# Performance work log

Hardware: AMD Instinct MI355X
Metric: run time of the kernel (lower is better)

The kernel has to match this reference:

```python
import jax, jax.numpy as jnp
import numpy as np

N = 50000      # num nodes
HID = 64       # hidden_dim
N2V = 64       # node2vec dim
E = 800000     # num edges
EP = 100000    # prediction edges
L = 2          # num_layers
EPS = 1e-5     # BatchNorm eps


def setup_inputs() -> dict:
    key = jax.random.key(0)
    ks = jax.random.split(key, 8)
    edge_index = jax.random.randint(ks[0], (2, E), 0, N)
    pred_edge = jax.random.randint(ks[1], (EP, 2), 0, N)
    id_emb = jax.random.normal(ks[2], (N, HID), jnp.float32) * 0.1      # learnable ID embedding
    n2v_emb = jax.random.normal(ks[3], (N, N2V), jnp.float32) * 0.1     # frozen node2vec embedding
    proj_w = jax.random.normal(ks[4], (HID + N2V, HID), jnp.float32) / np.sqrt(HID + N2V)
    proj_b = jnp.zeros((HID,), jnp.float32)
    conv_w = jax.random.normal(ks[5], (L, HID, HID), jnp.float32) / np.sqrt(HID)
    conv_b = jnp.zeros((L, HID), jnp.float32)
    bn_gamma = jnp.ones((L, HID), jnp.float32)
    bn_beta = jnp.zeros((L, HID), jnp.float32)
    return {"edge_index": edge_index, "pred_edge": pred_edge, "id_emb": id_emb,
            "n2v_emb": n2v_emb, "proj_w": proj_w, "proj_b": proj_b,
            "conv_w": conv_w, "conv_b": conv_b, "bn_gamma": bn_gamma, "bn_beta": bn_beta}


def reference(edge_index, pred_edge, id_emb, n2v_emb, proj_w, proj_b, conv_w, conv_b, bn_gamma, bn_beta):
    # input projection of concatenated embeddings: [N, HID+N2V] @ [HID+N2V, HID]
    x = jnp.concatenate([id_emb, n2v_emb], axis=1) @ proj_w + proj_b

    # GCN normalization with self-loops: norm_e = d^-1/2[src] * d^-1/2[dst]
    loops = jnp.arange(N, dtype=edge_index.dtype)
    row = jnp.concatenate([edge_index[0], loops])   # source nodes
    col = jnp.concatenate([edge_index[1], loops])   # destination nodes
    deg = jax.ops.segment_sum(jnp.ones(row.shape, x.dtype), col, num_segments=N)
    dis = jnp.where(deg > 0, jax.lax.rsqrt(deg), 0.0)
    norm = dis[row] * dis[col]                      # [E+N]

    for l in range(L):
        h = x @ conv_w[l]                                                    # [N, HID]
        agg = jax.ops.segment_sum(norm[:, None] * h[row], col, num_segments=N) + conv_b[l]
        # BatchNorm1d (training-mode batch stats over nodes)
        mu = agg.mean(axis=0)
        var = agg.var(axis=0)
        xn = (agg - mu) * jax.lax.rsqrt(var + EPS) * bn_gamma[l] + bn_beta[l]
        x = x + jax.nn.relu(xn)                                              # residual (shapes match)

    # dot-product link decoder
    z = x
    return (z[pred_edge[:, 0]] * z[pred_edge[:, 1]]).sum(axis=1)
```

## Files before the change

kernel.cpp:

```cpp
#include <hip/hip_runtime.h>

#define NN 50000
#define HID 64
#define NE 800000
#define NP 100000
#define BN_EPS 1e-5f
#define NB1 196

static inline size_t alignup(size_t x) { return (x + 255) & ~(size_t)255; }

__device__ __forceinline__ void f4fma(float a, const float4& w, float4& c) {
    c.x += a * w.x; c.y += a * w.y; c.z += a * w.z; c.w += a * w.w;
}
__device__ __forceinline__ void f4add(const float4& a, float4& c) {
    c.x += a.x; c.y += a.y; c.z += a.z; c.w += a.w;
}
__device__ __forceinline__ unsigned bfpack(float a, float b) {
    unsigned ua = __float_as_uint(a), ub = __float_as_uint(b);
    ua = (ua + 0x7fffu + ((ua >> 16) & 1u)) >> 16;
    ub = (ub + 0x7fffu + ((ub >> 16) & 1u)) >> 16;
    return ua | (ub << 16);
}
__device__ __forceinline__ float4 bf2f4(uint2 u) {
    float4 r;
    r.x = __uint_as_float(u.x << 16);
    r.y = __uint_as_float(u.x & 0xffff0000u);
    r.z = __uint_as_float(u.y << 16);
    r.w = __uint_as_float(u.y & 0xffff0000u);
    return r;
}


__global__ __launch_bounds__(256) void k_zero(int* __restrict__ cnt, float* __restrict__ sums,
                                              int* __restrict__ cursor) {
    int i = blockIdx.x * blockDim.x + threadIdx.x;
    if (i < NN) cnt[i] = 0;
    if (i < 256) sums[i] = 0.f;
    if (i == 0) *cursor = 0;
}


__global__ __launch_bounds__(256) void k_count(const int* __restrict__ col,
                                               int* __restrict__ cnt, int* __restrict__ rank) {
    int e = blockIdx.x * blockDim.x + threadIdx.x;
    if (e < NE) rank[e] = atomicAdd(&cnt[col[e]], 1);
}


__global__ __launch_bounds__(256) void k_alloc(const int* __restrict__ cnt,
                                               int* __restrict__ offs,
                                               float* __restrict__ dis,
                                               int* __restrict__ cursor) {
    __shared__ int s[256];
    __shared__ int base;
    int t = threadIdx.x;
    int i = blockIdx.x * 256 + t;
    int v = (i < NN) ? cnt[i] : 0;
    if (i < NN) dis[i] = rsqrtf((float)(v + 1));
    int va = (v + 7) & ~7;
    s[t] = va;
    __syncthreads();
    for (int off = 1; off < 256; off <<= 1) {
        int add = (t >= off) ? s[t - off] : 0;
        __syncthreads();
        s[t] += add;
        __syncthreads();
    }
    if (t == 255) base = atomicAdd(cursor, s[255]);
    __syncthreads();
    if (i < NN) offs[i] = base + s[t] - va;
}


__global__ __launch_bounds__(256) void k_fill(const int* __restrict__ row, const int* __restrict__ col,
                                              const int* __restrict__ rank, const int* __restrict__ offs,
                                              unsigned short* __restrict__ csr) {
    int e = blockIdx.x * blockDim.x + threadIdx.x;
    if (e >= NE) return;
    csr[offs[col[e]] + rank[e]] = (unsigned short)row[e];
}


__global__ __launch_bounds__(256) void k_proj(const float* __restrict__ id_emb,
                                              const float* __restrict__ n2v,
                                              const float* __restrict__ W,
                                              const float* __restrict__ b,
                                              const float* __restrict__ dis,
                                              float* __restrict__ x,
                                              unsigned short* __restrict__ xh) {
    __shared__ unsigned short Wlh[128 * 64];
    __shared__ unsigned short Al[32 * 132];
    int tid = threadIdx.x;
    int node0 = blockIdx.x * 32;
    const float2* W2f = (const float2*)W;
#pragma unroll
    for (int it = 0; it < 16; ++it) {
        int i = it * 256 + tid;
        float2 w = W2f[i];
        *(unsigned*)&Wlh[2 * i] = bfpack(w.x, w.y);
    }
    const float2* id2 = (const float2*)id_emb;
    const float2* nv2 = (const float2*)n2v;
#pragma unroll
    for (int it = 0; it < 8; ++it) {
        int i = it * 256 + tid;
        int r = i >> 6, kp = i & 63;
        int n = node0 + r;
        float2 v = make_float2(0.f, 0.f);
        if (n < NN) v = (kp < 32) ? id2[n * 32 + kp] : nv2[n * 32 + (kp - 32)];
        *(unsigned*)&Al[r * 132 + 2 * kp] = bfpack(v.x, v.y);
    }
    __syncthreads();
    int sub = tid >> 4, q = tid & 15;
    const uint2* W2 = (const uint2*)Wlh;
    float4* x4 = (float4*)x;
    uint2* xh2 = (uint2*)xh;
    float4 bb = ((const float4*)b)[q];
    float4 c0 = bb, c1 = bb;
#pragma unroll 4
    for (int k4 = 0; k4 < 32; ++k4) {
        float4 w0 = bf2f4(W2[(k4 * 4 + 0) * 16 + q]);
        float4 w1 = bf2f4(W2[(k4 * 4 + 1) * 16 + q]);
        float4 w2 = bf2f4(W2[(k4 * 4 + 2) * 16 + q]);
        float4 w3 = bf2f4(W2[(k4 * 4 + 3) * 16 + q]);
        float4 a0 = bf2f4(*(const uint2*)&Al[(sub * 2 + 0) * 132 + k4 * 4]);
        float4 a1 = bf2f4(*(const uint2*)&Al[(sub * 2 + 1) * 132 + k4 * 4]);
        f4fma(a0.x, w0, c0); f4fma(a0.y, w1, c0); f4fma(a0.z, w2, c0); f4fma(a0.w, w3, c0);
        f4fma(a1.x, w0, c1); f4fma(a1.y, w1, c1); f4fma(a1.z, w2, c1); f4fma(a1.w, w3, c1);
    }
    int n0 = node0 + sub * 2;
    if (n0 + 0 < NN) { float d = dis[n0+0]; x4[(n0+0)*16+q] = c0;
        xh2[(n0+0)*16+q] = make_uint2(bfpack(c0.x*d,c0.y*d), bfpack(c0.z*d,c0.w*d)); }
    if (n0 + 1 < NN) { float d = dis[n0+1]; x4[(n0+1)*16+q] = c1;
        xh2[(n0+1)*16+q] = make_uint2(bfpack(c1.x*d,c1.y*d), bfpack(c1.z*d,c1.w*d)); }
}


__global__ __launch_bounds__(256) void k_gather(const int* __restrict__ offs,
                                                const int* __restrict__ cnt,
                                                const unsigned short* __restrict__ csr,
                                                const float* __restrict__ dis,
                                                const unsigned short* __restrict__ xh,
                                                unsigned short* __restrict__ th) {
    int gw = (blockIdx.x * blockDim.x + threadIdx.x) >> 6;
    int lane = threadIdx.x & 63;
    int sub = lane >> 4, q = lane & 15;
    int node = gw * 4 + sub;
    if (node >= NN) return;
    const uint2* xh2 = (const uint2*)xh;
    float4 acc = make_float4(0.f, 0.f, 0.f, 0.f);
    const unsigned short* cs = csr + offs[node];
    int c = cnt[node];
    int jj = 0;
    for (; jj + 7 < c; jj += 8) {
        uint4 s8 = *(const uint4*)(cs + jj);
        int s0 = s8.x & 0xffff, s1 = s8.x >> 16;
        int s2 = s8.y & 0xffff, s3 = s8.y >> 16;
        int s4 = s8.z & 0xffff, s5 = s8.z >> 16;
        int s6 = s8.w & 0xffff, s7 = s8.w >> 16;
        uint2 u0 = xh2[s0 * 16 + q];
        uint2 u1 = xh2[s1 * 16 + q];
        uint2 u2 = xh2[s2 * 16 + q];
        uint2 u3 = xh2[s3 * 16 + q];
        uint2 u4 = xh2[s4 * 16 + q];
        uint2 u5 = xh2[s5 * 16 + q];
        uint2 u6 = xh2[s6 * 16 + q];
        uint2 u7 = xh2[s7 * 16 + q];
        f4add(bf2f4(u0), acc); f4add(bf2f4(u1), acc);
        f4add(bf2f4(u2), acc); f4add(bf2f4(u3), acc);
        f4add(bf2f4(u4), acc); f4add(bf2f4(u5), acc);
        f4add(bf2f4(u6), acc); f4add(bf2f4(u7), acc);
    }
    for (; jj < c; ++jj) {
        uint2 u0 = xh2[cs[jj] * 16 + q];
        f4add(bf2f4(u0), acc);
    }
    f4add(bf2f4(xh2[node * 16 + q]), acc);
    float di = dis[node];
    acc.x *= di; acc.y *= di; acc.z *= di; acc.w *= di;
    ((uint2*)th)[node * 16 + q] = make_uint2(bfpack(acc.x, acc.y), bfpack(acc.z, acc.w));
}


__global__ __launch_bounds__(256) void k_gemm_stats(const unsigned short* __restrict__ th,
                                                    const float* __restrict__ W,
                                                    float* __restrict__ agg,
                                                    float* __restrict__ sums) {
    __shared__ float Wl[64 * 64];
    __shared__ float ls0[16][64];
    __shared__ float ls1[16][64];
    int tid = threadIdx.x;
    for (int i = tid; i < 64 * 64; i += 256) Wl[i] = W[i];
    __syncthreads();
    int sub = tid >> 4, q = tid & 15;
    const uint2* t2 = (const uint2*)th;
    const float4* W4 = (const float4*)Wl;
    float4* agg4 = (float4*)agg;
    float4 s1 = make_float4(0.f, 0.f, 0.f, 0.f), s2 = s1;
    const int ngroups = (NN + 63) / 64;
    for (int g = blockIdx.x; g < ngroups; g += gridDim.x) {
        int n0 = g * 64 + sub * 4;
        int r0 = min(n0 + 0, NN - 1), r1 = min(n0 + 1, NN - 1);
        int r2 = min(n0 + 2, NN - 1), r3 = min(n0 + 3, NN - 1);
        float4 c0 = make_float4(0.f,0.f,0.f,0.f), c1 = c0, c2 = c0, c3 = c0;
#pragma unroll 4
        for (int k4 = 0; k4 < 16; ++k4) {
            float4 a0 = bf2f4(t2[r0 * 16 + k4]);
            float4 a1 = bf2f4(t2[r1 * 16 + k4]);
            float4 a2 = bf2f4(t2[r2 * 16 + k4]);
            float4 a3 = bf2f4(t2[r3 * 16 + k4]);
            float4 w0 = W4[(k4 * 4 + 0) * 16 + q];
            float4 w1 = W4[(k4 * 4 + 1) * 16 + q];
            float4 w2 = W4[(k4 * 4 + 2) * 16 + q];
            float4 w3 = W4[(k4 * 4 + 3) * 16 + q];
            f4fma(a0.x, w0, c0); f4fma(a0.y, w1, c0); f4fma(a0.z, w2, c0); f4fma(a0.w, w3, c0);
            f4fma(a1.x, w0, c1); f4fma(a1.y, w1, c1); f4fma(a1.z, w2, c1); f4fma(a1.w, w3, c1);
            f4fma(a2.x, w0, c2); f4fma(a2.y, w1, c2); f4fma(a2.z, w2, c2); f4fma(a2.w, w3, c2);
            f4fma(a3.x, w0, c3); f4fma(a3.y, w1, c3); f4fma(a3.z, w2, c3); f4fma(a3.w, w3, c3);
        }
        if (n0 + 0 < NN) { agg4[(n0 + 0) * 16 + q] = c0;
            s1.x += c0.x; s1.y += c0.y; s1.z += c0.z; s1.w += c0.w;
            s2.x += c0.x*c0.x; s2.y += c0.y*c0.y; s2.z += c0.z*c0.z; s2.w += c0.w*c0.w; }
        if (n0 + 1 < NN) { agg4[(n0 + 1) * 16 + q] = c1;
            s1.x += c1.x; s1.y += c1.y; s1.z += c1.z; s1.w += c1.w;
            s2.x += c1.x*c1.x; s2.y += c1.y*c1.y; s2.z += c1.z*c1.z; s2.w += c1.w*c1.w; }
        if (n0 + 2 < NN) { agg4[(n0 + 2) * 16 + q] = c2;
            s1.x += c2.x; s1.y += c2.y; s1.z += c2.z; s1.w += c2.w;
            s2.x += c2.x*c2.x; s2.y += c2.y*c2.y; s2.z += c2.z*c2.z; s2.w += c2.w*c2.w; }
        if (n0 + 3 < NN) { agg4[(n0 + 3) * 16 + q] = c3;
            s1.x += c3.x; s1.y += c3.y; s1.z += c3.z; s1.w += c3.w;
            s2.x += c3.x*c3.x; s2.y += c3.y*c3.y; s2.z += c3.z*c3.z; s2.w += c3.w*c3.w; }
    }
    ls0[sub][q * 4 + 0] = s1.x; ls0[sub][q * 4 + 1] = s1.y;
    ls0[sub][q * 4 + 2] = s1.z; ls0[sub][q * 4 + 3] = s1.w;
    ls1[sub][q * 4 + 0] = s2.x; ls1[sub][q * 4 + 1] = s2.y;
    ls1[sub][q * 4 + 2] = s2.z; ls1[sub][q * 4 + 3] = s2.w;
    __syncthreads();
    if (tid < 64) {
        float a = 0.f;
#pragma unroll
        for (int r = 0; r < 16; ++r) a += ls0[r][tid];
        atomicAdd(&sums[tid], a);
    } else if (tid < 128) {
        int c = tid - 64;
        float a = 0.f;
#pragma unroll
        for (int r = 0; r < 16; ++r) a += ls1[r][c];
        atomicAdd(&sums[64 + c], a);
    }
}


__global__ __launch_bounds__(256) void k_bnupdate(const float* __restrict__ agg,
                                                  const float* __restrict__ sums,
                                                  const float* __restrict__ gamma,
                                                  const float* __restrict__ beta,
                                                  const float* __restrict__ dis,
                                                  int prescale,
                                                  float* __restrict__ x,
                                                  unsigned short* __restrict__ xh) {
    int i = blockIdx.x * blockDim.x + threadIdx.x;
    if (i >= NN * 16) return;
    int f4 = i & 15;
    const float invn = 1.0f / (float)NN;
    float4 sm = ((const float4*)sums)[f4];
    float4 sq = ((const float4*)(sums + 64))[f4];
    float4 g = ((const float4*)gamma)[f4];
    float4 be = ((const float4*)beta)[f4];
    float4 a = ((const float4*)agg)[i];
    float4 xv = ((const float4*)x)[i];
    float mu, var, rstd, xn;
    mu = sm.x * invn; var = sq.x * invn - mu * mu; rstd = rsqrtf(var + BN_EPS);
    xn = (a.x - mu) * rstd * g.x + be.x; xv.x += fmaxf(xn, 0.f);
    mu = sm.y * invn; var = sq.y * invn - mu * mu; rstd = rsqrtf(var + BN_EPS);
    xn = (a.y - mu) * rstd * g.y + be.y; xv.y += fmaxf(xn, 0.f);
    mu = sm.z * invn; var = sq.z * invn - mu * mu; rstd = rsqrtf(var + BN_EPS);
    xn = (a.z - mu) * rstd * g.z + be.z; xv.z += fmaxf(xn, 0.f);
    mu = sm.w * invn; var = sq.w * invn - mu * mu; rstd = rsqrtf(var + BN_EPS);
    xn = (a.w - mu) * rstd * g.w + be.w; xv.w += fmaxf(xn, 0.f);
    ((float4*)x)[i] = xv;
    float d = prescale ? dis[i >> 4] : 1.0f;
    ((uint2*)xh)[i] = make_uint2(bfpack(xv.x * d, xv.y * d), bfpack(xv.z * d, xv.w * d));
}


__global__ __launch_bounds__(256) void k_decode(const int* __restrict__ pred,
                                                const unsigned short* __restrict__ zh,
                                                float* __restrict__ out) {
    int gw = (blockIdx.x * blockDim.x + threadIdx.x) >> 6;
    int lane = threadIdx.x & 63;
    int sub = lane >> 4, q = lane & 15;
    int p = gw * 4 + sub;
    if (p >= NP) return;
    const uint2* z2 = (const uint2*)zh;
    int a = pred[2 * p], b = pred[2 * p + 1];
    float4 va = bf2f4(z2[a * 16 + q]);
    float4 vb = bf2f4(z2[b * 16 + q]);
    float v = va.x * vb.x + va.y * vb.y + va.z * vb.z + va.w * vb.w;
    v += __shfl_xor(v, 1);
    v += __shfl_xor(v, 2);
    v += __shfl_xor(v, 4);
    v += __shfl_xor(v, 8);
    if (q == 0) out[p] = v;
}

extern "C" void kernel_launch(void* const* d_in, const int* in_sizes, int n_in,
                              void* d_out, int out_size, void* d_ws, size_t ws_size,
                              hipStream_t stream) {
    const int* edge_index = (const int*)d_in[0];
    const int* pred       = (const int*)d_in[1];
    const float* id_emb   = (const float*)d_in[2];
    const float* n2v      = (const float*)d_in[3];
    const float* proj_w   = (const float*)d_in[4];
    const float* proj_b   = (const float*)d_in[5];
    const float* conv_w   = (const float*)d_in[6];
    const float* gamma    = (const float*)d_in[8];
    const float* beta     = (const float*)d_in[9];
    float* out = (float*)d_out;

    char* ws = (char*)d_ws;
    size_t off = 0;
    float* dis   = (float*)(ws + off); off += alignup(NN * 4);
    int* cnt     = (int*)(ws + off);   off += alignup(NN * 4);
    int* offs    = (int*)(ws + off);   off += alignup(NN * 4);
    int* rank    = (int*)(ws + off);   off += alignup((size_t)NE * 4);
    int* cursor  = (int*)(ws + off);   off += alignup(4);
    unsigned short* csr = (unsigned short*)(ws + off); off += alignup((size_t)(NE + NN * 8) * 2);
    float* x     = (float*)(ws + off); off += alignup((size_t)NN * 64 * 4);
    float* agg   = (float*)(ws + off); off += alignup((size_t)NN * 64 * 4);
    unsigned short* xh = (unsigned short*)(ws + off); off += alignup((size_t)NN * 64 * 2);
    unsigned short* th = (unsigned short*)(ws + off); off += alignup((size_t)NN * 64 * 2);
    float* sums  = (float*)(ws + off);

    const int* row = edge_index;
    const int* col = edge_index + NE;

    k_zero<<<NB1, 256, 0, stream>>>(cnt, sums, cursor);
    k_count<<<(NE + 255) / 256, 256, 0, stream>>>(col, cnt, rank);
    k_alloc<<<NB1, 256, 0, stream>>>(cnt, offs, dis, cursor);
    k_fill<<<(NE + 255) / 256, 256, 0, stream>>>(row, col, rank, offs, csr);

    k_proj<<<(NN + 31) / 32, 256, 0, stream>>>(id_emb, n2v, proj_w, proj_b, dis, x, xh);

    for (int l = 0; l < 2; ++l) {
        k_gather<<<((NN + 3) / 4 * 64 + 255) / 256, 256, 0, stream>>>(offs, cnt, csr, dis, xh, th);
        k_gemm_stats<<<512, 256, 0, stream>>>(th, conv_w + l * 64 * 64, agg, sums + l * 128);
        k_bnupdate<<<(NN * 16 + 255) / 256, 256, 0, stream>>>(agg, sums + l * 128, gamma + l * 64,
                                                              beta + l * 64, dis, (l == 0) ? 1 : 0, x, xh);
    }

    k_decode<<<(NP / 4 * 64 + 255) / 256, 256, 0, stream>>>(pred, xh, out);
}
```

Baseline: 201.7 us.

## Fuse GEMM, BatchNorm stats and update via grid-wide barrier

Merges the GEMM+stats kernel and the BN update kernel into one. It launches one block per 64-node group (782 blocks) and uses an atomic counter spin barrier so that all blocks wait for the global column sums before applying BatchNorm. The GEMM results stay in registers, which removes the fp32 agg buffer write and read and one kernel launch per layer. The cost is the grid-wide barrier. It deadlocks unless all 782 blocks are co-resident, so the code depends on occupancy (launch_bounds 256,4) and has no fallback.

```diff
diff --git a/kernel.cpp b/kernel.cpp
--- a/kernel.cpp
+++ b/kernel.cpp
@@ -6,6 +6,7 @@
 #define NP 100000
 #define BN_EPS 1e-5f
 #define NB1 196
+#define NGRP ((NN + 63) / 64)
 
 static inline size_t alignup(size_t x) { return (x + 255) & ~(size_t)255; }
 
@@ -32,11 +33,12 @@
 
 
 __global__ __launch_bounds__(256) void k_zero(int* __restrict__ cnt, float* __restrict__ sums,
-                                              int* __restrict__ cursor) {
+                                              int* __restrict__ cursor, unsigned* __restrict__ done) {
     int i = blockIdx.x * blockDim.x + threadIdx.x;
     if (i < NN) cnt[i] = 0;
     if (i < 256) sums[i] = 0.f;
     if (i == 0) *cursor = 0;
+    if (i < 2) done[i] = 0u;
 }
 
 
@@ -182,10 +184,16 @@
 }
 
 
-__global__ __launch_bounds__(256) void k_gemm_stats(const unsigned short* __restrict__ th,
-                                                    const float* __restrict__ W,
-                                                    float* __restrict__ agg,
-                                                    float* __restrict__ sums) {
+__global__ __launch_bounds__(256, 4) void k_gemmbn(const unsigned short* __restrict__ th,
+                                                   const float* __restrict__ W,
+                                                   float* __restrict__ sums,
+                                                   unsigned* __restrict__ done,
+                                                   const float* __restrict__ gamma,
+                                                   const float* __restrict__ beta,
+                                                   const float* __restrict__ dis,
+                                                   int prescale,
+                                                   float* __restrict__ x,
+                                                   unsigned short* __restrict__ xh) {
     __shared__ float Wl[64 * 64];
     __shared__ float ls0[16][64];
     __shared__ float ls1[16][64];
@@ -195,42 +203,34 @@
     int sub = tid >> 4, q = tid & 15;
     const uint2* t2 = (const uint2*)th;
     const float4* W4 = (const float4*)Wl;
-    float4* agg4 = (float4*)agg;
-    float4 s1 = make_float4(0.f, 0.f, 0.f, 0.f), s2 = s1;
-    const int ngroups = (NN + 63) / 64;
-    for (int g = blockIdx.x; g < ngroups; g += gridDim.x) {
-        int n0 = g * 64 + sub * 4;
-        int r0 = min(n0 + 0, NN - 1), r1 = min(n0 + 1, NN - 1);
-        int r2 = min(n0 + 2, NN - 1), r3 = min(n0 + 3, NN - 1);
-        float4 c0 = make_float4(0.f,0.f,0.f,0.f), c1 = c0, c2 = c0, c3 = c0;
+    int n0 = blockIdx.x * 64 + sub * 4;
+    int r0 = min(n0 + 0, NN - 1), r1 = min(n0 + 1, NN - 1);
+    int r2 = min(n0 + 2, NN - 1), r3 = min(n0 + 3, NN - 1);
+    float4 c0 = make_float4(0.f,0.f,0.f,0.f), c1 = c0, c2 = c0, c3 = c0;
 #pragma unroll 4
-        for (int k4 = 0; k4 < 16; ++k4) {
-            float4 a0 = bf2f4(t2[r0 * 16 + k4]);
-            float4 a1 = bf2f4(t2[r1 * 16 + k4]);
-            float4 a2 = bf2f4(t2[r2 * 16 + k4]);
-            float4 a3 = bf2f4(t2[r3 * 16 + k4]);
-            float4 w0 = W4[(k4 * 4 + 0) * 16 + q];
-            float4 w1 = W4[(k4 * 4 + 1) * 16 + q];
-            float4 w2 = W4[(k4 * 4 + 2) * 16 + q];
-            float4 w3 = W4[(k4 * 4 + 3) * 16 + q];
-            f4fma(a0.x, w0, c0); f4fma(a0.y, w1, c0); f4fma(a0.z, w2, c0); f4fma(a0.w, w3, c0);
-            f4fma(a1.x, w0, c1); f4fma(a1.y, w1, c1); f4fma(a1.z, w2, c1); f4fma(a1.w, w3, c1);
-            f4fma(a2.x, w0, c2); f4fma(a2.y, w1, c2); f4fma(a2.z, w2, c2); f4fma(a2.w, w3, c2);
-            f4fma(a3.x, w0, c3); f4fma(a3.y, w1, c3); f4fma(a3.z, w2, c3); f4fma(a3.w, w3, c3);
-        }
-        if (n0 + 0 < NN) { agg4[(n0 + 0) * 16 + q] = c0;
-            s1.x += c0.x; s1.y += c0.y; s1.z += c0.z; s1.w += c0.w;
-            s2.x += c0.x*c0.x; s2.y += c0.y*c0.y; s2.z += c0.z*c0.z; s2.w += c0.w*c0.w; }
-        if (n0 + 1 < NN) { agg4[(n0 + 1) * 16 + q] = c1;
-            s1.x += c1.x; s1.y += c1.y; s1.z += c1.z; s1.w += c1.w;
-            s2.x += c1.x*c1.x; s2.y += c1.y*c1.y; s2.z += c1.z*c1.z; s2.w += c1.w*c1.w; }
-        if (n0 + 2 < NN) { agg4[(n0 + 2) * 16 + q] = c2;
-            s1.x += c2.x; s1.y += c2.y; s1.z += c2.z; s1.w += c2.w;
-            s2.x += c2.x*c2.x; s2.y += c2.y*c2.y; s2.z += c2.z*c2.z; s2.w += c2.w*c2.w; }
-        if (n0 + 3 < NN) { agg4[(n0 + 3) * 16 + q] = c3;
-            s1.x += c3.x; s1.y += c3.y; s1.z += c3.z; s1.w += c3.w;
-            s2.x += c3.x*c3.x; s2.y += c3.y*c3.y; s2.z += c3.z*c3.z; s2.w += c3.w*c3.w; }
-    }
+    for (int k4 = 0; k4 < 16; ++k4) {
+        float4 a0 = bf2f4(t2[r0 * 16 + k4]);
+        float4 a1 = bf2f4(t2[r1 * 16 + k4]);
+        float4 a2 = bf2f4(t2[r2 * 16 + k4]);
+        float4 a3 = bf2f4(t2[r3 * 16 + k4]);
+        float4 w0 = W4[(k4 * 4 + 0) * 16 + q];
+        float4 w1 = W4[(k4 * 4 + 1) * 16 + q];
+        float4 w2 = W4[(k4 * 4 + 2) * 16 + q];
+        float4 w3 = W4[(k4 * 4 + 3) * 16 + q];
+        f4fma(a0.x, w0, c0); f4fma(a0.y, w1, c0); f4fma(a0.z, w2, c0); f4fma(a0.w, w3, c0);
+        f4fma(a1.x, w0, c1); f4fma(a1.y, w1, c1); f4fma(a1.z, w2, c1); f4fma(a1.w, w3, c1);
+        f4fma(a2.x, w0, c2); f4fma(a2.y, w1, c2); f4fma(a2.z, w2, c2); f4fma(a2.w, w3, c2);
+        f4fma(a3.x, w0, c3); f4fma(a3.y, w1, c3); f4fma(a3.z, w2, c3); f4fma(a3.w, w3, c3);
+    }
+    float4 s1 = make_float4(0.f,0.f,0.f,0.f), s2 = s1;
+    if (n0 + 0 < NN) { s1.x += c0.x; s1.y += c0.y; s1.z += c0.z; s1.w += c0.w;
+        s2.x += c0.x*c0.x; s2.y += c0.y*c0.y; s2.z += c0.z*c0.z; s2.w += c0.w*c0.w; }
+    if (n0 + 1 < NN) { s1.x += c1.x; s1.y += c1.y; s1.z += c1.z; s1.w += c1.w;
+        s2.x += c1.x*c1.x; s2.y += c1.y*c1.y; s2.z += c1.z*c1.z; s2.w += c1.w*c1.w; }
+    if (n0 + 2 < NN) { s1.x += c2.x; s1.y += c2.y; s1.z += c2.z; s1.w += c2.w;
+        s2.x += c2.x*c2.x; s2.y += c2.y*c2.y; s2.z += c2.z*c2.z; s2.w += c2.w*c2.w; }
+    if (n0 + 3 < NN) { s1.x += c3.x; s1.y += c3.y; s1.z += c3.z; s1.w += c3.w;
+        s2.x += c3.x*c3.x; s2.y += c3.y*c3.y; s2.z += c3.z*c3.z; s2.w += c3.w*c3.w; }
     ls0[sub][q * 4 + 0] = s1.x; ls0[sub][q * 4 + 1] = s1.y;
     ls0[sub][q * 4 + 2] = s1.z; ls0[sub][q * 4 + 3] = s1.w;
     ls1[sub][q * 4 + 0] = s2.x; ls1[sub][q * 4 + 1] = s2.y;
@@ -248,39 +248,50 @@
         for (int r = 0; r < 16; ++r) a += ls1[r][c];
         atomicAdd(&sums[64 + c], a);
     }
-}
-
-
-__global__ __launch_bounds__(256) void k_bnupdate(const float* __restrict__ agg,
-                                                  const float* __restrict__ sums,
-                                                  const float* __restrict__ gamma,
-                                                  const float* __restrict__ beta,
-                                                  const float* __restrict__ dis,
-                                                  int prescale,
-                                                  float* __restrict__ x,
-                                                  unsigned short* __restrict__ xh) {
-    int i = blockIdx.x * blockDim.x + threadIdx.x;
-    if (i >= NN * 16) return;
-    int f4 = i & 15;
+    __syncthreads();
+    if (tid == 0) {
+        __threadfence();
+        __hip_atomic_fetch_add(done, 1u, __ATOMIC_ACQ_REL, __HIP_MEMORY_SCOPE_AGENT);
+        while (__hip_atomic_load(done, __ATOMIC_ACQUIRE, __HIP_MEMORY_SCOPE_AGENT) < (unsigned)NGRP)
+            __builtin_amdgcn_s_sleep(8);
+    }
+    __syncthreads();
     const float invn = 1.0f / (float)NN;
-    float4 sm = ((const float4*)sums)[f4];
-    float4 sq = ((const float4*)(sums + 64))[f4];
-    float4 g = ((const float4*)gamma)[f4];
-    float4 be = ((const float4*)beta)[f4];
-    float4 a = ((const float4*)agg)[i];
-    float4 xv = ((const float4*)x)[i];
-    float mu, var, rstd, xn;
-    mu = sm.x * invn; var = sq.x * invn - mu * mu; rstd = rsqrtf(var + BN_EPS);
-    xn = (a.x - mu) * rstd * g.x + be.x; xv.x += fmaxf(xn, 0.f);
-    mu = sm.y * invn; var = sq.y * invn - mu * mu; rstd = rsqrtf(var + BN_EPS);
-    xn = (a.y - mu) * rstd * g.y + be.y; xv.y += fmaxf(xn, 0.f);
-    mu = sm.z * invn; var = sq.z * invn - mu * mu; rstd = rsqrtf(var + BN_EPS);
-    xn = (a.z - mu) * rstd * g.z + be.z; xv.z += fmaxf(xn, 0.f);
-    mu = sm.w * invn; var = sq.w * invn - mu * mu; rstd = rsqrtf(var + BN_EPS);
-    xn = (a.w - mu) * rstd * g.w + be.w; xv.w += fmaxf(xn, 0.f);
-    ((float4*)x)[i] = xv;
-    float d = prescale ? dis[i >> 4] : 1.0f;
-    ((uint2*)xh)[i] = make_uint2(bfpack(xv.x * d, xv.y * d), bfpack(xv.z * d, xv.w * d));
+    float mu0, mu1, mu2, mu3, rs0, rs1, rs2, rs3, sm, sq, var;
+    sm = __hip_atomic_load(&sums[q * 4 + 0], __ATOMIC_RELAXED, __HIP_MEMORY_SCOPE_AGENT);
+    sq = __hip_atomic_load(&sums[64 + q * 4 + 0], __ATOMIC_RELAXED, __HIP_MEMORY_SCOPE_AGENT);
+    mu0 = sm * invn; var = sq * invn - mu0 * mu0; rs0 = rsqrtf(var + BN_EPS);
+    sm = __hip_atomic_load(&sums[q * 4 + 1], __ATOMIC_RELAXED, __HIP_MEMORY_SCOPE_AGENT);
+    sq = __hip_atomic_load(&sums[64 + q * 4 + 1], __ATOMIC_RELAXED, __HIP_MEMORY_SCOPE_AGENT);
+    mu1 = sm * invn; var = sq * invn - mu1 * mu1; rs1 = rsqrtf(var + BN_EPS);
+    sm = __hip_atomic_load(&sums[q * 4 + 2], __ATOMIC_RELAXED, __HIP_MEMORY_SCOPE_AGENT);
+    sq = __hip_atomic_load(&sums[64 + q * 4 + 2], __ATOMIC_RELAXED, __HIP_MEMORY_SCOPE_AGENT);
+    mu2 = sm * invn; var = sq * invn - mu2 * mu2; rs2 = rsqrtf(var + BN_EPS);
+    sm = __hip_atomic_load(&sums[q * 4 + 3], __ATOMIC_RELAXED, __HIP_MEMORY_SCOPE_AGENT);
+    sq = __hip_atomic_load(&sums[64 + q * 4 + 3], __ATOMIC_RELAXED, __HIP_MEMORY_SCOPE_AGENT);
+    mu3 = sm * invn; var = sq * invn - mu3 * mu3; rs3 = rsqrtf(var + BN_EPS);
+    float4 g4 = ((const float4*)gamma)[q];
+    float4 be4 = ((const float4*)beta)[q];
+    float4* x4 = (float4*)x;
+    uint2* xh2 = (uint2*)xh;
+#define BN_ROW(ci, idx)                                                                 \
+    if (n0 + idx < NN) {                                                                \
+        float4 xv = x4[(n0 + idx) * 16 + q];                                            \
+        float xn;                                                                       \
+        xn = (ci.x - mu0) * rs0 * g4.x + be4.x; xv.x += fmaxf(xn, 0.f);                 \
+        xn = (ci.y - mu1) * rs1 * g4.y + be4.y; xv.y += fmaxf(xn, 0.f);                 \
+        xn = (ci.z - mu2) * rs2 * g4.z + be4.z; xv.z += fmaxf(xn, 0.f);                 \
+        xn = (ci.w - mu3) * rs3 * g4.w + be4.w; xv.w += fmaxf(xn, 0.f);                 \
+        x4[(n0 + idx) * 16 + q] = xv;                                                   \
+        float d = prescale ? dis[n0 + idx] : 1.0f;                                      \
+        xh2[(n0 + idx) * 16 + q] = make_uint2(bfpack(xv.x * d, xv.y * d),               \
+                                              bfpack(xv.z * d, xv.w * d));              \
+    }
+    BN_ROW(c0, 0)
+    BN_ROW(c1, 1)
+    BN_ROW(c2, 2)
+    BN_ROW(c3, 3)
+#undef BN_ROW
 }
 
 
@@ -325,9 +336,9 @@
     int* offs    = (int*)(ws + off);   off += alignup(NN * 4);
     int* rank    = (int*)(ws + off);   off += alignup((size_t)NE * 4);
     int* cursor  = (int*)(ws + off);   off += alignup(4);
+    unsigned* done = (unsigned*)(ws + off); off += alignup(8);
     unsigned short* csr = (unsigned short*)(ws + off); off += alignup((size_t)(NE + NN * 8) * 2);
     float* x     = (float*)(ws + off); off += alignup((size_t)NN * 64 * 4);
-    float* agg   = (float*)(ws + off); off += alignup((size_t)NN * 64 * 4);
     unsigned short* xh = (unsigned short*)(ws + off); off += alignup((size_t)NN * 64 * 2);
     unsigned short* th = (unsigned short*)(ws + off); off += alignup((size_t)NN * 64 * 2);
     float* sums  = (float*)(ws + off);
@@ -335,7 +346,7 @@
     const int* row = edge_index;
     const int* col = edge_index + NE;
 
-    k_zero<<<NB1, 256, 0, stream>>>(cnt, sums, cursor);
+    k_zero<<<NB1, 256, 0, stream>>>(cnt, sums, cursor, done);
     k_count<<<(NE + 255) / 256, 256, 0, stream>>>(col, cnt, rank);
     k_alloc<<<NB1, 256, 0, stream>>>(cnt, offs, dis, cursor);
     k_fill<<<(NE + 255) / 256, 256, 0, stream>>>(row, col, rank, offs, csr);
@@ -344,9 +355,8 @@
 
     for (int l = 0; l < 2; ++l) {
         k_gather<<<((NN + 3) / 4 * 64 + 255) / 256, 256, 0, stream>>>(offs, cnt, csr, dis, xh, th);
-        k_gemm_stats<<<512, 256, 0, stream>>>(th, conv_w + l * 64 * 64, agg, sums + l * 128);
-        k_bnupdate<<<(NN * 16 + 255) / 256, 256, 0, stream>>>(agg, sums + l * 128, gamma + l * 64,
-                                                              beta + l * 64, dis, (l == 0) ? 1 : 0, x, xh);
+        k_gemmbn<<<NGRP, 256, 0, stream>>>(th, conv_w + l * 64 * 64, sums + l * 128, done + l,
+                                           gamma + l * 64, beta + l * 64, dis, (l == 0) ? 1 : 0, x, xh);
     }
 
     k_decode<<<(NP / 4 * 64 + 255) / 256, 256, 0, stream>>>(pred, xh, out);
```

After: 388.1 us. 92.4% more time.
